# Performance work log

Measured on AMD Instinct MI355X. Metric: run time of the kernel, lower is better.

The kernel has to match this reference:

```python
import jax, jax.numpy as jnp
import numpy as np

B, S, E = 4, 2048, 1024
H = 16
D = E // H
WIN = 512


def setup_inputs() -> dict:
    key = jax.random.key(0)
    k1, k2, k3 = jax.random.split(key, 3)
    x = jax.random.normal(k1, (B, S, E), dtype=jnp.float32)
    w_in = jax.random.normal(k2, (3 * E, E), dtype=jnp.float32) * 0.02
    w_out = jax.random.normal(k3, (E, E), dtype=jnp.float32) * 0.02
    return {"x": x, "w_in": w_in, "w_out": w_out}


def _sliding_window_attention(q, k, v, win):
    b, h, s, d = q.shape
    nb = s // win
    scale = 1.0 / jnp.sqrt(jnp.float32(d))
    qb = q.reshape(b, h, nb, win, d)
    kb = k.reshape(b, h, nb, win, d)
    vb = v.reshape(b, h, nb, win, d)
    zpad = jnp.zeros_like(kb[:, :, :1])
    k2 = jnp.concatenate([jnp.concatenate([zpad, kb[:, :, :-1]], axis=2), kb], axis=3)  # [B,H,nb,2W,D]
    v2 = jnp.concatenate([jnp.concatenate([zpad, vb[:, :, :-1]], axis=2), vb], axis=3)
    scores = jnp.einsum('bhnqd,bhnkd->bhnqk', qb, k2) * scale  # [B,H,nb,W,2W]
    qi = jnp.arange(win)[:, None]          # query offset in block
    kj = jnp.arange(2 * win)[None, :]
    delta = qi - kj + win                  # q_idx - kv_idx
    valid = (delta >= 0) & (delta <= win)  # sliding-window causal mask
    blk = jnp.arange(nb)[:, None, None]
    valid = valid[None] & (blk * win + (kj[None] - win) >= 0)  # prev block invalid for block 0
    # ALiBi: bias = (q_idx - kv_idx) * exp2(-(h+1)*8/H)
    slopes = jnp.exp2(-(jnp.arange(H, dtype=jnp.float32) + 1.0) * 8.0 / H)  # [H]
    bias = slopes[:, None, None] * delta.astype(jnp.float32)  # [H,W,2W]
    scores = jnp.where(valid[None, :, :, :, :][:, None].squeeze(0)[None] if False else valid[None, None],
                       scores + bias[None, :, None], -jnp.inf)
    p = jax.nn.softmax(scores, axis=-1)
    out = jnp.einsum('bhnqk,bhnkd->bhnqd', p, v2)
    return out.reshape(b, h, s, d)


def reference(x, w_in, w_out):
    b, s, e = x.shape
    # packed in-projection (q is k is v path): split [3E,E] weight
    qkv = jnp.einsum('bse,fe->bsf', x, w_in)  # [B,S,3E]
    q, k, v = jnp.split(qkv, 3, axis=-1)
    def heads(t):
        return t.reshape(b, s, H, D).transpose(0, 2, 1, 3)  # [B,H,S,D]
    o = _sliding_window_attention(heads(q), heads(k), heads(v), WIN)  # [B,H,S,D]
    o = o.transpose(0, 2, 1, 3).reshape(b, s, e)
    return jnp.einsum('bse,fe->bsf', o, w_out)  # out_proj, batch-first output
```

## Files before the change

kernel.cpp:

```cpp
#include <hip/hip_runtime.h>
#include <hip/hip_bf16.h>


typedef __bf16 bf16x8 __attribute__((ext_vector_type(8)));
typedef __bf16 bf16x4 __attribute__((ext_vector_type(4)));
typedef short short4v __attribute__((ext_vector_type(4)));
typedef float f32x4 __attribute__((ext_vector_type(4)));

__device__ __forceinline__ f32x4 mfma16(bf16x8 a, bf16x8 b, f32x4 c) {
    return __builtin_amdgcn_mfma_f32_16x16x32_bf16(a, b, c, 0, 0, 0);
}

__device__ __forceinline__ f32x4 mfma16k16(bf16x4 a, bf16x4 b, f32x4 c) {
#if __has_builtin(__builtin_amdgcn_mfma_f32_16x16x16bf16_1k)
    return __builtin_amdgcn_mfma_f32_16x16x16bf16_1k(
        __builtin_bit_cast(short4v, a), __builtin_bit_cast(short4v, b), c, 0, 0, 0);
#elif __has_builtin(__builtin_amdgcn_mfma_f32_16x16x16_bf16)
    return __builtin_amdgcn_mfma_f32_16x16x16_bf16(a, b, c, 0, 0, 0);
#else
    asm("v_mfma_f32_16x16x16_bf16 %0, %1, %2, %0" : "+v"(c) : "v"(a), "v"(b));
    return c;
#endif
}

__device__ __forceinline__ void gload_lds16(const void* g, void* l) {
    __builtin_amdgcn_global_load_lds(
        (const __attribute__((address_space(1))) unsigned int*)(unsigned long long)g,
        (__attribute__((address_space(3))) unsigned int*)(unsigned int)(unsigned long long)l,
        16, 0, 0);
}

__device__ __forceinline__ unsigned pkbf(float a, float b) {
    unsigned short ua = __builtin_bit_cast(unsigned short, (__bf16)a);
    unsigned short ub = __builtin_bit_cast(unsigned short, (__bf16)b);
    return (unsigned)ua | ((unsigned)ub << 16);
}

__global__ void init_flag(int* flag) { *flag = 0; }

__global__ void detect_f32(const unsigned short* __restrict__ w, int n, int* flag) {
    int i = blockIdx.x * blockDim.x + threadIdx.x;
    int hit = 0;
    for (; i < n; i += gridDim.x * blockDim.x) {
        int e = (w[i] >> 7) & 0xFF;
        if (e >= 0x8D) hit = 1;
    }
    unsigned long long m = __ballot(hit);
    if (m != 0 && (threadIdx.x & 63) == 0) atomicOr(flag, 1);
}

__global__ void cvt_all(const void* __restrict__ x, const void* __restrict__ wi,
                        const void* __restrict__ wo, __bf16* __restrict__ xb,
                        __bf16* __restrict__ wib, __bf16* __restrict__ wob,
                        const int* __restrict__ flag) {
    if (*flag == 0) return;
    const int XN = 8192 * 1024, WI = 3072 * 1024, WO = 1024 * 1024;
    const int stride = gridDim.x * blockDim.x;
    int i0 = blockIdx.x * blockDim.x + threadIdx.x;
    for (int j = i0; j < XN; j += stride) xb[j] = (__bf16)((const float*)x)[j];
    for (int j = i0; j < WI; j += stride) wib[j] = (__bf16)((const float*)wi)[j];
    for (int j = i0; j < WO; j += stride) wob[j] = (__bf16)((const float*)wo)[j];
}

__global__ __launch_bounds__(256, 3) void gemm_bt(
        const void* __restrict__ Araw, const __bf16* __restrict__ Acvt,
        const void* __restrict__ Braw, const __bf16* __restrict__ Bcvt,
        __bf16* __restrict__ Cb, float* __restrict__ Cf,
        const int* __restrict__ flagp, int M, int N, int K) {
    __shared__ __align__(16) __bf16 As[128 * 64];
    __shared__ __align__(16) __bf16 Bs[128 * 64];

    const int t = threadIdx.x;
    const int lane = t & 63;
    const int w = t >> 6;
    const int wr = w >> 1, wc = w & 1;
    const int q4 = lane >> 4, l16 = lane & 15;
    const int m0 = blockIdx.y * 128, n0 = blockIdx.x * 128;
    const bool isf32 = (*flagp != 0);
    const __bf16* A = isf32 ? Acvt : (const __bf16*)Araw;
    const __bf16* Bt = isf32 ? Bcvt : (const __bf16*)Braw;

    f32x4 acc[4][4] = {};

    const int lr = lane >> 3;
    const int lc = (lane & 7) ^ lr;

    for (int k0 = 0; k0 < K; k0 += 64) {
#pragma unroll
        for (int p = 0; p < 4; ++p) {
            int r0 = w * 32 + p * 8;
            gload_lds16(&A[(size_t)(m0 + r0 + lr) * K + k0 + lc * 8], &As[r0 * 64]);
            gload_lds16(&Bt[(size_t)(n0 + r0 + lr) * K + k0 + lc * 8], &Bs[r0 * 64]);
        }
        __syncthreads();

#pragma unroll
        for (int kt = 0; kt < 2; ++kt) {
            bf16x8 af[4], bfr[4];
#pragma unroll
            for (int mt = 0; mt < 4; ++mt) {
                int row = wr * 64 + mt * 16 + l16;
                af[mt] = *(const bf16x8*)&As[row * 64 + (((kt * 4 + q4) ^ (row & 7)) << 3)];
            }
#pragma unroll
            for (int nt = 0; nt < 4; ++nt) {
                int row = wc * 64 + nt * 16 + l16;
                bfr[nt] = *(const bf16x8*)&Bs[row * 64 + (((kt * 4 + q4) ^ (row & 7)) << 3)];
            }
#pragma unroll
            for (int mt = 0; mt < 4; ++mt)
#pragma unroll
                for (int nt = 0; nt < 4; ++nt)
                    acc[mt][nt] = mfma16(af[mt], bfr[nt], acc[mt][nt]);
        }
        __syncthreads();
    }

#pragma unroll
    for (int mt = 0; mt < 4; ++mt)
#pragma unroll
        for (int nt = 0; nt < 4; ++nt) {
            int col = n0 + wc * 64 + nt * 16 + l16;
#pragma unroll
            for (int r = 0; r < 4; ++r) {
                int row = m0 + wr * 64 + mt * 16 + q4 * 4 + r;
                if (Cf && isf32)
                    Cf[(size_t)row * N + col] = acc[mt][nt][r];
                else
                    Cb[(size_t)row * N + col] = (__bf16)acc[mt][nt][r];
            }
        }
}

__global__ __launch_bounds__(256, 2) void attn(
        const __bf16* __restrict__ qkv, __bf16* __restrict__ o) {
    __shared__ __align__(16) char smem[2 * 16384 + 2 * 17408];
    __bf16* Ks  = (__bf16*)smem;
    __bf16* Vts = (__bf16*)(smem + 32768);
    __bf16* Ot  = (__bf16*)smem;

    const int L = blockIdx.x;
    const int u = L & 255, v = L >> 8;
    const int qt = v * 4 + (u & 3);
    const int h  = (u >> 2) & 15;
    const int b  = u >> 6;

    const int t = threadIdx.x;
    const int lane = t & 63, w = t >> 6;
    const int q4 = lane >> 4, l16 = lane & 15;
    const int q0 = qt * 128, qw0 = q0 + w * 32;

    const float L2E = 1.4426950408889634f;
    const float slope2 = exp2f(-(float)(h + 1) * 0.5f) * L2E;
    const float scale2 = L2E * 0.125f;

    const int srow = t >> 3, scb = t & 7;
    const int lr = lane >> 3;
    const int lc = (lane & 7) ^ lr;

    bf16x8 qf[2][2];
    const size_t qbase = ((size_t)b * 2048 + q0) * 3072 + (size_t)h * 64;
#pragma unroll
    for (int nt = 0; nt < 2; ++nt)
#pragma unroll
        for (int kt = 0; kt < 2; ++kt)
            qf[nt][kt] = *(const bf16x8*)&qkv[qbase +
                (size_t)(w * 32 + nt * 16 + l16) * 3072 + kt * 32 + q4 * 8];

    f32x4 O[4][2] = {};
    float mrow[2] = {-1e30f, -1e30f}, lrow[2] = {0.0f, 0.0f};

    const int nkt = (qt < 4 ? qt : 4) + 1;
    const int ktile0 = qt - (nkt - 1);
    const size_t bh = (size_t)b * 2048 * 3072 + (size_t)h * 64;

    uint4 vpre[4];

    {
        const size_t kb = bh + (size_t)(ktile0 * 128) * 3072 + 1024;
#pragma unroll
        for (int p = 0; p < 4; ++p) {
            int r0 = w * 32 + p * 8;
            gload_lds16(&qkv[kb + (size_t)(r0 + lr) * 3072 + lc * 8], &Ks[r0 * 64]);
        }
#pragma unroll
        for (int p = 0; p < 4; ++p)
            vpre[p] = *(const uint4*)&qkv[kb + 1024 + (size_t)(p * 32 + srow) * 3072 + scb * 8];
#pragma unroll
        for (int p = 0; p < 4; ++p) {
            const __bf16* ve = (const __bf16*)&vpre[p];
            int R = p * 4 + (srow >> 3);
#pragma unroll
            for (int j = 0; j < 8; ++j)
                Vts[(scb * 8 + j) * 136 + ((R ^ scb) << 3) + (srow & 7)] = ve[j];
        }
    }
    __syncthreads();

    for (int ki = 0; ki < nkt; ++ki) {
        const int k0 = (ktile0 + ki) * 128;
        const __bf16* Kb = Ks + (ki & 1) * 8192;
        const __bf16* Vb = Vts + (ki & 1) * 8704;
        if (ki + 1 < nkt) {
            const size_t kb = bh + (size_t)(k0 + 128) * 3072 + 1024;
            __bf16* Kn = Ks + ((ki + 1) & 1) * 8192;
#pragma unroll
            for (int p = 0; p < 4; ++p) {
                int r0 = w * 32 + p * 8;
                gload_lds16(&qkv[kb + (size_t)(r0 + lr) * 3072 + lc * 8], &Kn[r0 * 64]);
            }
#pragma unroll
            for (int p = 0; p < 4; ++p)
                vpre[p] = *(const uint4*)&qkv[kb + 1024 + (size_t)(p * 32 + srow) * 3072 + scb * 8];
        }

#pragma unroll 1
        for (int hh = 0; hh < 2; ++hh) {
            const int ks0 = k0 + hh * 64;
            if (qw0 + 31 < ks0 || qw0 - 512 > ks0 + 63) continue;
            const bool interior = (qw0 - ks0 >= 63) && (qw0 - ks0 <= 481);

            f32x4 sc[2][4] = {};
#pragma unroll
            for (int mt = 0; mt < 4; ++mt) {
                int krow = hh * 64 + mt * 16 + l16;
                bf16x8 ak0 = *(const bf16x8*)&Kb[krow * 64 + ((q4 ^ (l16 & 7)) << 3)];
                bf16x8 ak1 = *(const bf16x8*)&Kb[krow * 64 + (((4 + q4) ^ (l16 & 7)) << 3)];
                __builtin_amdgcn_s_setprio(1);
                sc[0][mt] = mfma16(ak0, qf[0][0], sc[0][mt]);
                sc[0][mt] = mfma16(ak1, qf[0][1], sc[0][mt]);
                sc[1][mt] = mfma16(ak0, qf[1][0], sc[1][mt]);
                sc[1][mt] = mfma16(ak1, qf[1][1], sc[1][mt]);
                __builtin_amdgcn_s_setprio(0);
            }

            uint2 pb[2][4];

#pragma unroll
            for (int nt = 0; nt < 2; ++nt) {
                const int qi = qw0 + nt * 16 + l16;
                const int db = qi - ks0 - q4 * 4;
                float tmx = -1e30f;
                if (interior) {
                    const float fb = slope2 * (float)db;
#pragma unroll
                    for (int mt = 0; mt < 4; ++mt) {
                        float bm = fb - (float)(16 * mt) * slope2;
#pragma unroll
                        for (int r = 0; r < 4; ++r) {
                            float v = fmaf(sc[nt][mt][r], scale2, bm - (float)r * slope2);
                            sc[nt][mt][r] = v;
                            tmx = fmaxf(tmx, v);
                        }
                    }
                } else {
#pragma unroll
                    for (int mt = 0; mt < 4; ++mt)
#pragma unroll
                        for (int r = 0; r < 4; ++r) {
                            int delta = db - mt * 16 - r;
                            float v = sc[nt][mt][r] * scale2 + slope2 * (float)delta;
                            v = ((unsigned)delta <= 512u) ? v : -1e30f;
                            sc[nt][mt][r] = v;
                            tmx = fmaxf(tmx, v);
                        }
                }
                tmx = fmaxf(tmx, __shfl_xor(tmx, 16));
                tmx = fmaxf(tmx, __shfl_xor(tmx, 32));

                if (__any(tmx > mrow[nt])) {
                    float mnew = fmaxf(mrow[nt], tmx);
                    float al = exp2f(mrow[nt] - mnew);
                    mrow[nt] = mnew;
                    lrow[nt] *= al;
#pragma unroll
                    for (int mtd = 0; mtd < 4; ++mtd)
                        O[mtd][nt] *= al;
                }

                float rs = 0.0f;
#pragma unroll
                for (int mt = 0; mt < 4; ++mt) {
                    float p0 = exp2f(sc[nt][mt][0] - mrow[nt]);
                    float p1 = exp2f(sc[nt][mt][1] - mrow[nt]);
                    float p2 = exp2f(sc[nt][mt][2] - mrow[nt]);
                    float p3 = exp2f(sc[nt][mt][3] - mrow[nt]);
                    rs += (p0 + p1) + (p2 + p3);
                    uint2 pk;
                    pk.x = pkbf(p0, p1);
                    pk.y = pkbf(p2, p3);
                    pb[nt][mt] = pk;
                }
                rs += __shfl_xor(rs, 16);
                rs += __shfl_xor(rs, 32);
                lrow[nt] += rs;
            }

            const int dsw = l16 >> 3;
#pragma unroll
            for (int mtB = 0; mtB < 4; ++mtB) {
                bf16x4 b0 = __builtin_bit_cast(bf16x4, pb[0][mtB]);
                bf16x4 b1 = __builtin_bit_cast(bf16x4, pb[1][mtB]);
                const int kc0 = hh * 8 + mtB * 2 + (q4 >> 1);
#pragma unroll
                for (int mtd = 0; mtd < 4; ++mtd) {
                    int kc = kc0 ^ ((mtd * 2 + dsw) & 7);
                    bf16x4 av = *(const bf16x4*)&Vb[(mtd * 16 + l16) * 136 +
                                                    (kc << 3) + (q4 & 1) * 4];
                    __builtin_amdgcn_s_setprio(1);
                    O[mtd][0] = mfma16k16(av, b0, O[mtd][0]);
                    O[mtd][1] = mfma16k16(av, b1, O[mtd][1]);
                    __builtin_amdgcn_s_setprio(0);
                }
            }
        }

        if (ki + 1 < nkt) {
            __bf16* Vn = Vts + ((ki + 1) & 1) * 8704;
#pragma unroll
            for (int p = 0; p < 4; ++p) {
                const __bf16* ve = (const __bf16*)&vpre[p];
                int R = p * 4 + (srow >> 3);
#pragma unroll
                for (int j = 0; j < 8; ++j)
                    Vn[(scb * 8 + j) * 136 + ((R ^ scb) << 3) + (srow & 7)] = ve[j];
            }
        }
        __syncthreads();
    }

#pragma unroll
    for (int nt = 0; nt < 2; ++nt) {
        float inv = (lrow[nt] > 0.0f) ? 1.0f / lrow[nt] : 0.0f;
        int qrow = w * 32 + nt * 16 + l16;
#pragma unroll
        for (int mtd = 0; mtd < 4; ++mtd) {
            int chunk = (mtd * 2 + (q4 >> 1)) ^ (l16 & 7);
            uint2 pk;
            pk.x = pkbf(O[mtd][nt][0] * inv, O[mtd][nt][1] * inv);
            pk.y = pkbf(O[mtd][nt][2] * inv, O[mtd][nt][3] * inv);
            *(uint2*)&Ot[qrow * 64 + (chunk << 3) + (q4 & 1) * 4] = pk;
        }
    }
    const size_t obase = ((size_t)b * 2048 + q0) * 1024 + (size_t)h * 64;
#pragma unroll
    for (int i = 0; i < 4; ++i) {
        int u2 = i * 64 + lane;
        int row = u2 >> 3, ch = u2 & 7;
        int q = w * 32 + row;
        *(uint4*)&o[obase + (size_t)q * 1024 + ch * 8] =
            *(const uint4*)&Ot[q * 64 + ((ch ^ (row & 7)) << 3)];
    }
}

extern "C" void kernel_launch(void* const* d_in, const int* in_sizes, int n_in,
                              void* d_out, int out_size, void* d_ws, size_t ws_size,
                              hipStream_t stream) {
    char* ws = (char*)d_ws;
    int* flag = (int*)ws;
    size_t off = 256;
    __bf16* xb  = (__bf16*)(ws + off); off += (size_t)8192 * 1024 * 2;
    __bf16* wib = (__bf16*)(ws + off); off += (size_t)3072 * 1024 * 2;
    __bf16* wob = (__bf16*)(ws + off); off += (size_t)1024 * 1024 * 2;
    __bf16* qkv = (__bf16*)(ws + off); off += (size_t)8192 * 3072 * 2;
    __bf16* o   = (__bf16*)(ws + off);

    init_flag<<<1, 1, 0, stream>>>(flag);
    int nscan = in_sizes[2] < 65536 ? in_sizes[2] : 65536;
    detect_f32<<<16, 256, 0, stream>>>((const unsigned short*)d_in[2], nscan, flag);
    cvt_all<<<1024, 256, 0, stream>>>(d_in[0], d_in[1], d_in[2], xb, wib, wob, flag);

    gemm_bt<<<dim3(24, 64), 256, 0, stream>>>(d_in[0], xb, d_in[1], wib,
                                              qkv, nullptr, flag, 8192, 3072, 1024);
    attn<<<dim3(1024), 256, 0, stream>>>(qkv, o);
    gemm_bt<<<dim3(8, 64), 256, 0, stream>>>(o, o, d_in[2], wob,
                                             (__bf16*)d_out, (float*)d_out, flag,
                                             8192, 1024, 1024);
}
```

Measured before the change: 263.8 us.

## Vectorize fp32-to-bf16 conversion and remap GEMM workgroups across XCDs

The conversion kernel now reads float4 and writes four packed bf16 values per iteration instead of one scalar per thread, which cuts load/store instruction count. The GEMM remaps the linear workgroup id so that consecutive tiles land on the same XCD chiplet, aiming for better L2 reuse of A/B tiles. The remap assumes the workgroup count is divisible by 8 and relies on a pkbf helper defined elsewhere.

```diff
diff --git a/kernel.cpp b/kernel.cpp
--- a/kernel.cpp
+++ b/kernel.cpp
@@ -54,12 +54,27 @@
                         __bf16* __restrict__ wib, __bf16* __restrict__ wob,
                         const int* __restrict__ flag) {
     if (*flag == 0) return;
-    const int XN = 8192 * 1024, WI = 3072 * 1024, WO = 1024 * 1024;
+    const int XN = 8192 * 1024 / 4, WI = 3072 * 1024 / 4, WO = 1024 * 1024 / 4;
     const int stride = gridDim.x * blockDim.x;
-    int i0 = blockIdx.x * blockDim.x + threadIdx.x;
-    for (int j = i0; j < XN; j += stride) xb[j] = (__bf16)((const float*)x)[j];
-    for (int j = i0; j < WI; j += stride) wib[j] = (__bf16)((const float*)wi)[j];
-    for (int j = i0; j < WO; j += stride) wob[j] = (__bf16)((const float*)wo)[j];
+    const int i0 = blockIdx.x * blockDim.x + threadIdx.x;
+    const float4* xs = (const float4*)x;
+    const float4* ws1 = (const float4*)wi;
+    const float4* ws2 = (const float4*)wo;
+    for (int j = i0; j < XN; j += stride) {
+        float4 v = xs[j];
+        uint2 pk; pk.x = pkbf(v.x, v.y); pk.y = pkbf(v.z, v.w);
+        *(uint2*)&xb[(size_t)j * 4] = pk;
+    }
+    for (int j = i0; j < WI; j += stride) {
+        float4 v = ws1[j];
+        uint2 pk; pk.x = pkbf(v.x, v.y); pk.y = pkbf(v.z, v.w);
+        *(uint2*)&wib[(size_t)j * 4] = pk;
+    }
+    for (int j = i0; j < WO; j += stride) {
+        float4 v = ws2[j];
+        uint2 pk; pk.x = pkbf(v.x, v.y); pk.y = pkbf(v.z, v.w);
+        *(uint2*)&wob[(size_t)j * 4] = pk;
+    }
 }
 
 __global__ __launch_bounds__(256, 3) void gemm_bt(
@@ -75,7 +90,14 @@
     const int w = t >> 6;
     const int wr = w >> 1, wc = w & 1;
     const int q4 = lane >> 4, l16 = lane & 15;
-    const int m0 = blockIdx.y * 128, n0 = blockIdx.x * 128;
+
+    const int nwg = gridDim.x * gridDim.y;
+    const int lin = blockIdx.y * gridDim.x + blockIdx.x;
+    const int slin = (lin & 7) * (nwg >> 3) + (lin >> 3);
+    const int bx = slin % gridDim.x;
+    const int by = slin / gridDim.x;
+    const int m0 = by * 128, n0 = bx * 128;
+
     const bool isf32 = (*flagp != 0);
     const __bf16* A = isf32 ? Acvt : (const __bf16*)Araw;
     const __bf16* Bt = isf32 ? Bcvt : (const __bf16*)Braw;
```

Result: faster. 246.9 us (-6.4%).
